# Performance work log

Hardware: AMD Instinct MI355X
Metric: run time of the kernel (lower is better)

## Reference

```python
import jax, jax.numpy as jnp
import numpy as np
from jax import lax

N_INPUTS = 8
N_OUTPUTS = 4
N_RESERVOIR = 2048
T = 4096
SPECTRAL_RADIUS = 0.95
NOISE = 0.001


def setup_inputs() -> dict:
    key = jax.random.key(0)
    ks = jax.random.split(key, 8)
    inputs = jax.random.normal(ks[0], (T, N_INPUTS), dtype=jnp.float32)
    outputs = jax.random.normal(ks[1], (T, N_OUTPUTS), dtype=jnp.float32)
    # recurrent weights: uniform(-0.5, 0.5), rescaled to spectral radius ~0.95.
    # For a uniform(-0.5,0.5) NxN matrix the spectral radius is ~ sqrt(N/12)
    # (circular law), used here in place of an explicit eigendecomposition.
    w_raw = jax.random.uniform(ks[2], (N_RESERVOIR, N_RESERVOIR), dtype=jnp.float32) - 0.5
    radius = jnp.sqrt(N_RESERVOIR / 12.0)
    w = w_raw * (SPECTRAL_RADIUS / radius)
    w_in = jax.random.uniform(ks[3], (N_RESERVOIR, N_INPUTS), dtype=jnp.float32) * 2.0 - 1.0
    w_feedb = jax.random.uniform(ks[4], (N_RESERVOIR, N_OUTPUTS), dtype=jnp.float32) * 2.0 - 1.0
    # readout (nn.Linear): weight [n_out, R+n_in], bias [n_out]
    fan_in = N_RESERVOIR + N_INPUTS
    bound = 1.0 / np.sqrt(fan_in)
    lin_w = jax.random.uniform(ks[5], (N_OUTPUTS, fan_in), dtype=jnp.float32, minval=-bound, maxval=bound)
    lin_b = jax.random.uniform(ks[6], (N_OUTPUTS,), dtype=jnp.float32, minval=-bound, maxval=bound)
    # per-step regularization noise: noise * (uniform - 0.5), pre-drawn for determinism
    noise_seq = NOISE * (jax.random.uniform(ks[7], (T, N_RESERVOIR), dtype=jnp.float32) - 0.5)
    return {"inputs": inputs, "outputs": outputs, "w": w, "w_in": w_in,
            "w_feedb": w_feedb, "lin_w": lin_w, "lin_b": lin_b, "noise_seq": noise_seq}


def reference(inputs, outputs, w, w_in, w_feedb, lin_w, lin_b, noise_seq):
    # Echo-state recurrence: x_n = tanh(w @ x_{n-1} + w_in @ u_n + w_feedb @ y_{n-1}) + noise_n
    # States row 0 stays zero (original loop starts at n=1).
    R = w.shape[0]

    def step(x, per_step):
        u_n, y_prev, nz = per_step
        x_new = jnp.tanh(w @ x + w_in @ u_n + w_feedb @ y_prev) + nz
        return x_new, x_new

    x0 = jnp.zeros((R,), dtype=inputs.dtype)
    _, xs = lax.scan(step, x0, (inputs[1:], outputs[:-1], noise_seq[1:]))  # [T-1, R]

    zero_row_x = jnp.zeros((1, R), dtype=inputs.dtype)
    zero_row_u = jnp.zeros((1, inputs.shape[1]), dtype=inputs.dtype)
    states_x = jnp.concatenate([zero_row_x, xs], axis=0)              # [T, R]
    states_u = jnp.concatenate([zero_row_u, inputs[1:]], axis=0)       # [T, n_in]
    states = jnp.concatenate([states_x, states_u], axis=1)             # [T, R+n_in]

    out = states @ lin_w.T + lin_b                                     # [T, n_out]
    return out
```

## Files before the change

kernel.cpp:

```cpp
#include <hip/hip_runtime.h>

#define T_STEPS 4096
#define RSIZE   2048
#define N_IN    8
#define N_OUT   4
#define NWG     256
#define NT      256
#define LIN_STRIDE  (RSIZE + N_IN)
#define SENTINEL    0x7FC00000u

typedef float v4 __attribute__((ext_vector_type(4)));
typedef float v2 __attribute__((ext_vector_type(2)));


__global__ __launch_bounds__(256) void init_kernel(v4* __restrict__ states4) {
    int idx = blockIdx.x * 256 + threadIdx.x;
    const float s = __uint_as_float(SENTINEL);
    v4 v = (idx < RSIZE / 4) ? (v4){0.f, 0.f, 0.f, 0.f} : (v4){s, s, s, s};
    states4[idx] = v;
}

__device__ __forceinline__ float dot4(v4 a, v4 b) {
    float s = a.x * b.x;
    s = fmaf(a.y, b.y, s);
    s = fmaf(a.z, b.z, s);
    s = fmaf(a.w, b.w, s);
    return s;
}


__global__ __launch_bounds__(NT, 1) void reservoir_kernel(
    const float* __restrict__ W,
    const float* __restrict__ Win,
    const float* __restrict__ Wfb,
    const float* __restrict__ inputs,
    const float* __restrict__ outputs,
    const float* __restrict__ noise,
    float* __restrict__ states)
{
    const int g    = blockIdx.x;
    const int t    = threadIdx.x;
    const int lane = t & 63;
    const int wv   = t >> 6;
    const int wid  = g * 4 + wv;
    const int r0   = wid * 2;

    const float* wr0 = W + (size_t)r0 * RSIZE + lane * 8;
    const float* wr1 = wr0 + RSIZE;
    v4 w000 = *(const v4*)(wr0 +    0), w001 = *(const v4*)(wr0 +    4);
    v4 w010 = *(const v4*)(wr0 +  512), w011 = *(const v4*)(wr0 +  516);
    v4 w020 = *(const v4*)(wr0 + 1024), w021 = *(const v4*)(wr0 + 1028);
    v4 w030 = *(const v4*)(wr0 + 1536), w031 = *(const v4*)(wr0 + 1540);
    v4 w100 = *(const v4*)(wr1 +    0), w101 = *(const v4*)(wr1 +    4);
    v4 w110 = *(const v4*)(wr1 +  512), w111 = *(const v4*)(wr1 +  516);
    v4 w120 = *(const v4*)(wr1 + 1024), w121 = *(const v4*)(wr1 + 1028);
    v4 w130 = *(const v4*)(wr1 + 1536), w131 = *(const v4*)(wr1 + 1540);
    asm volatile("" : "+v"(w000), "+v"(w001), "+v"(w010), "+v"(w011));
    asm volatile("" : "+v"(w020), "+v"(w021), "+v"(w030), "+v"(w031));
    asm volatile("" : "+v"(w100), "+v"(w101), "+v"(w110), "+v"(w111));
    asm volatile("" : "+v"(w120), "+v"(w121), "+v"(w130), "+v"(w131));

    float win[N_IN] = {0}, wfb[N_OUT] = {0};
    if (lane < 2) {
        const int r = r0 + lane;
        #pragma unroll
        for (int j = 0; j < N_IN; ++j)  win[j] = Win[r * N_IN + j];
        #pragma unroll
        for (int k = 0; k < N_OUT; ++k) wfb[k] = Wfb[r * N_OUT + k];
    }

    __shared__ v4 xsh[2][RSIZE / 4];
    const int e     = lane * 2;
    const int sx    = e ^ ((e >> 3) & 7);
    const int fillc = wv * 512 + lane * 8;
    const int fbase = wv * 128;

    for (int n = 1; n < T_STEPS; ++n) {
        float pre = 0.0f, nz = 0.0f;
        if (lane < 2) {
            const int r = r0 + lane;
            nz = noise[(size_t)n * RSIZE + r];
            #pragma unroll
            for (int j = 0; j < N_IN; ++j)  pre = fmaf(win[j], inputs[n * N_IN + j], pre);
            #pragma unroll
            for (int k = 0; k < N_OUT; ++k) pre = fmaf(wfb[k], outputs[(n - 1) * N_OUT + k], pre);
        }

        const volatile v4* src =
            (const volatile v4*)(states + (size_t)(n - 1) * RSIZE + fillc);
        v4 a, b;
        for (;;) {
            a = src[0];
            b = src[1];
            bool ok = (__float_as_uint(a.x) != SENTINEL) &
                      (__float_as_uint(a.y) != SENTINEL) &
                      (__float_as_uint(a.z) != SENTINEL) &
                      (__float_as_uint(a.w) != SENTINEL) &
                      (__float_as_uint(b.x) != SENTINEL) &
                      (__float_as_uint(b.y) != SENTINEL) &
                      (__float_as_uint(b.z) != SENTINEL) &
                      (__float_as_uint(b.w) != SENTINEL);
            if (ok) break;
            __builtin_amdgcn_s_sleep(1);
        }

        const int p = (n - 1) & 1;
        xsh[p][fbase + sx]       = a;
        xsh[p][fbase + (sx ^ 1)] = b;
        __syncthreads();

        float acc0 = 0.0f, acc1 = 0.0f;
        {
            v4 x0 = xsh[p][  0 + sx], x1 = xsh[p][  0 + (sx ^ 1)];
            acc0 += dot4(w000, x0) + dot4(w001, x1);
            acc1 += dot4(w100, x0) + dot4(w101, x1);
        }
        {
            v4 x0 = xsh[p][128 + sx], x1 = xsh[p][128 + (sx ^ 1)];
            acc0 += dot4(w010, x0) + dot4(w011, x1);
            acc1 += dot4(w110, x0) + dot4(w111, x1);
        }
        {
            v4 x0 = xsh[p][256 + sx], x1 = xsh[p][256 + (sx ^ 1)];
            acc0 += dot4(w020, x0) + dot4(w021, x1);
            acc1 += dot4(w120, x0) + dot4(w121, x1);
        }
        {
            v4 x0 = xsh[p][384 + sx], x1 = xsh[p][384 + (sx ^ 1)];
            acc0 += dot4(w030, x0) + dot4(w031, x1);
            acc1 += dot4(w130, x0) + dot4(w131, x1);
        }

        #pragma unroll
        for (int m = 1; m < 64; m <<= 1) {
            acc0 += __shfl_xor(acc0, m, 64);
            acc1 += __shfl_xor(acc1, m, 64);
        }

        float xn = 0.0f;
        if (lane < 2) {
            float s = (lane == 0 ? acc0 : acc1) + pre;
            xn = tanhf(s) + nz;
        }
        float xn1 = __shfl(xn, 1, 64);
        if (lane == 0) {
            v2 st; st.x = xn; st.y = xn1;
            *(volatile v2*)(states + (size_t)n * RSIZE + r0) = st;
        }
        __builtin_amdgcn_s_waitcnt(0);
    }
}

__global__ __launch_bounds__(256) void readout_kernel(
    const float* __restrict__ states,
    const float* __restrict__ inputs,
    const float* __restrict__ lin_w,
    const float* __restrict__ lin_b,
    float* __restrict__ out)
{
    const int ti   = blockIdx.x;
    const int tid  = threadIdx.x;
    const int lane = tid & 63;
    const int wave = tid >> 6;
    const int c0   = tid * 8;

    const float* xp = states + (size_t)ti * RSIZE + c0;
    v4 xa = *(const v4*)xp;
    v4 xb = *(const v4*)(xp + 4);

    float acc[N_OUT];
    #pragma unroll
    for (int o = 0; o < N_OUT; ++o) {
        const float* lp = lin_w + (size_t)o * LIN_STRIDE + c0;
        v4 la = *(const v4*)lp;
        v4 lb = *(const v4*)(lp + 4);
        acc[o] = dot4(la, xa) + dot4(lb, xb);
    }

    #pragma unroll
    for (int m = 1; m < 64; m <<= 1) {
        #pragma unroll
        for (int o = 0; o < N_OUT; ++o) acc[o] += __shfl_xor(acc[o], m, 64);
    }

    __shared__ float red[4][N_OUT];
    if (lane == 0) {
        #pragma unroll
        for (int o = 0; o < N_OUT; ++o) red[wave][o] = acc[o];
    }
    __syncthreads();

    if (tid < N_OUT) {
        float s = red[0][tid] + red[1][tid] + red[2][tid] + red[3][tid] + lin_b[tid];
        if (ti > 0) {
            #pragma unroll
            for (int j = 0; j < N_IN; ++j)
                s = fmaf(lin_w[(size_t)tid * LIN_STRIDE + RSIZE + j],
                         inputs[ti * N_IN + j], s);
        }
        out[ti * N_OUT + tid] = s;
    }
}

extern "C" void kernel_launch(void* const* d_in, const int* in_sizes, int n_in,
                              void* d_out, int out_size, void* d_ws, size_t ws_size,
                              hipStream_t stream) {
    const float* inputs  = (const float*)d_in[0];
    const float* outputs = (const float*)d_in[1];
    const float* W       = (const float*)d_in[2];
    const float* Win     = (const float*)d_in[3];
    const float* Wfb     = (const float*)d_in[4];
    const float* lin_w   = (const float*)d_in[5];
    const float* lin_b   = (const float*)d_in[6];
    const float* noise   = (const float*)d_in[7];
    float* out = (float*)d_out;

    float* states = (float*)d_ws;

    hipLaunchKernelGGL(init_kernel, dim3((T_STEPS * RSIZE / 4) / 256), dim3(256), 0,
                       stream, (v4*)states);
    hipLaunchKernelGGL(reservoir_kernel, dim3(NWG), dim3(NT), 0, stream,
                       W, Win, Wfb, inputs, outputs, noise, states);
    hipLaunchKernelGGL(readout_kernel, dim3(T_STEPS), dim3(256), 0, stream,
                       states, inputs, lin_w, lin_b, out);
}
```

Baseline: 7.112 ms.

## Have each wave poll the full state row directly instead of sharing via LDS

Each wave now reads all 2048 previous-state values it needs straight from global memory (volatile loads with sentinel checks) instead of each wave filling a quarter into shared memory and syncing the workgroup. This removes the __syncthreads barrier and LDS round trip from every recurrence step, so waves proceed independently. In exchange, global/L2 read traffic per step rises fourfold per workgroup, and each wave spins on the entire row, which can lengthen polling latency.

Measured after the change: 16.67 ms. +134.4%, slower.

```diff
diff --git a/kernel.cpp b/kernel.cpp
--- a/kernel.cpp
+++ b/kernel.cpp
@@ -69,11 +69,7 @@
         for (int k = 0; k < N_OUT; ++k) wfb[k] = Wfb[r * N_OUT + k];
     }
 
-    __shared__ v4 xsh[2][RSIZE / 4];
-    const int e     = lane * 2;
-    const int sx    = e ^ ((e >> 3) & 7);
-    const int fillc = wv * 512 + lane * 8;
-    const int fbase = wv * 128;
+    const int li = lane * 2;
 
     for (int n = 1; n < T_STEPS; ++n) {
         float pre = 0.0f, nz = 0.0f;
@@ -86,50 +82,33 @@
             for (int k = 0; k < N_OUT; ++k) pre = fmaf(wfb[k], outputs[(n - 1) * N_OUT + k], pre);
         }
 
-        const volatile v4* src =
-            (const volatile v4*)(states + (size_t)(n - 1) * RSIZE + fillc);
-        v4 a, b;
+        const volatile v4* row = (const volatile v4*)(states + (size_t)(n - 1) * RSIZE);
+        v4 x00, x01, x10, x11, x20, x21, x30, x31;
+        #define OKV(v) ((__float_as_uint(v.x) != SENTINEL) & \
+                        (__float_as_uint(v.y) != SENTINEL) & \
+                        (__float_as_uint(v.z) != SENTINEL) & \
+                        (__float_as_uint(v.w) != SENTINEL))
         for (;;) {
-            a = src[0];
-            b = src[1];
-            bool ok = (__float_as_uint(a.x) != SENTINEL) &
-                      (__float_as_uint(a.y) != SENTINEL) &
-                      (__float_as_uint(a.z) != SENTINEL) &
-                      (__float_as_uint(a.w) != SENTINEL) &
-                      (__float_as_uint(b.x) != SENTINEL) &
-                      (__float_as_uint(b.y) != SENTINEL) &
-                      (__float_as_uint(b.z) != SENTINEL) &
-                      (__float_as_uint(b.w) != SENTINEL);
+            x00 = row[  0 + li]; x01 = row[  0 + li + 1];
+            x10 = row[128 + li]; x11 = row[128 + li + 1];
+            x20 = row[256 + li]; x21 = row[256 + li + 1];
+            x30 = row[384 + li]; x31 = row[384 + li + 1];
+            bool ok = OKV(x00) & OKV(x01) & OKV(x10) & OKV(x11) &
+                      OKV(x20) & OKV(x21) & OKV(x30) & OKV(x31);
             if (ok) break;
             __builtin_amdgcn_s_sleep(1);
         }
-
-        const int p = (n - 1) & 1;
-        xsh[p][fbase + sx]       = a;
-        xsh[p][fbase + (sx ^ 1)] = b;
-        __syncthreads();
+        #undef OKV
 
         float acc0 = 0.0f, acc1 = 0.0f;
-        {
-            v4 x0 = xsh[p][  0 + sx], x1 = xsh[p][  0 + (sx ^ 1)];
-            acc0 += dot4(w000, x0) + dot4(w001, x1);
-            acc1 += dot4(w100, x0) + dot4(w101, x1);
-        }
-        {
-            v4 x0 = xsh[p][128 + sx], x1 = xsh[p][128 + (sx ^ 1)];
-            acc0 += dot4(w010, x0) + dot4(w011, x1);
-            acc1 += dot4(w110, x0) + dot4(w111, x1);
-        }
-        {
-            v4 x0 = xsh[p][256 + sx], x1 = xsh[p][256 + (sx ^ 1)];
-            acc0 += dot4(w020, x0) + dot4(w021, x1);
-            acc1 += dot4(w120, x0) + dot4(w121, x1);
-        }
-        {
-            v4 x0 = xsh[p][384 + sx], x1 = xsh[p][384 + (sx ^ 1)];
-            acc0 += dot4(w030, x0) + dot4(w031, x1);
-            acc1 += dot4(w130, x0) + dot4(w131, x1);
-        }
+        acc0 += dot4(w000, x00) + dot4(w001, x01);
+        acc1 += dot4(w100, x00) + dot4(w101, x01);
+        acc0 += dot4(w010, x10) + dot4(w011, x11);
+        acc1 += dot4(w110, x10) + dot4(w111, x11);
+        acc0 += dot4(w020, x20) + dot4(w021, x21);
+        acc1 += dot4(w120, x20) + dot4(w121, x21);
+        acc0 += dot4(w030, x30) + dot4(w031, x31);
+        acc1 += dot4(w130, x30) + dot4(w131, x31);
 
         #pragma unroll
         for (int m = 1; m < 64; m <<= 1) {
```
